# Optimization experiments

Measured on AMD Instinct MI355X. Metric: run time of the kernel, lower is better.

Reference implementation:

```python
import jax, jax.numpy as jnp
import numpy as np
from jax import lax

B, C, T, S = 32, 122, 500, 13
WID, EMB, PROJ = 80, 8, 1024
HID = 768  # (H=1)*(W=96)*(E=8) after CNN
EPS = 1e-5
DN = ('NCHW', 'OIHW', 'NCHW')


def setup_inputs() -> dict:
    key = jax.random.key(0)
    ks = jax.random.split(key, 24)
    f32 = jnp.float32
    def n(k, shape, scale):
        return (jax.random.normal(k, shape, dtype=f32) * scale).astype(f32)
    return {
        'x': jax.random.normal(ks[0], (B, C, T), dtype=f32),
        'subject_ids': jax.random.randint(ks[1], (B,), 0, S, dtype=jnp.int32),
        'W_sub': n(ks[2], (S, T, T), 0.04),      # nn.Linear(500,500) weight per subject
        'b_sub': n(ks[3], (S, T), 0.02),
        'conv1_w': n(ks[4], (WID, 1, 1, 5), 0.3),
        'conv1_b': n(ks[5], (WID,), 0.02),
        'bn1_g': 1.0 + n(ks[6], (WID,), 0.1),
        'bn1_b': n(ks[7], (WID,), 0.1),
        'bn1_m': n(ks[8], (WID,), 0.1),
        'bn1_v': 0.5 + jax.random.uniform(ks[9], (WID,), dtype=f32),
        'conv2_w': n(ks[10], (WID, WID, C, 1), 0.01),
        'conv2_b': n(ks[11], (WID,), 0.02),
        'bn2_g': 1.0 + n(ks[12], (WID,), 0.1),
        'bn2_b': n(ks[13], (WID,), 0.1),
        'bn2_m': n(ks[14], (WID,), 0.1),
        'bn2_v': 0.5 + jax.random.uniform(ks[15], (WID,), dtype=f32),
        'proj_w': n(ks[16], (EMB, WID, 1, 1), 0.1),
        'proj_b': n(ks[17], (EMB,), 0.02),
        'mlp1_w': n(ks[18], (PROJ, HID), 0.03),
        'mlp1_b': n(ks[19], (PROJ,), 0.02),
        'mlp2_w': n(ks[20], (PROJ, PROJ), 0.03),
        'mlp2_b': n(ks[21], (PROJ,), 0.02),
        'ln_g': 1.0 + n(ks[22], (PROJ,), 0.05),
        'ln_b': n(ks[23], (PROJ,), 0.05),
    }


def _bn(h, g, b, m, v):
    # eval-mode BatchNorm2d over channel axis 1
    scale = (g / jnp.sqrt(v + EPS))[None, :, None, None]
    shift = (b - m * g / jnp.sqrt(v + EPS))[None, :, None, None]
    return h * scale + shift


def _forward(x, subject_ids, W_sub, b_sub, conv1_w, conv1_b, bn1_g, bn1_b, bn1_m, bn1_v,
             conv2_w, conv2_b, bn2_g, bn2_b, bn2_m, bn2_v, proj_w, proj_b,
             mlp1_w, mlp1_b, mlp2_w, mlp2_b, ln_g, ln_b):
    # --- per-subject routing: gather each sample's Linear(500,500) and apply ---
    Wg = W_sub[subject_ids]                       # [B,T,T] (out,in)
    bg = b_sub[subject_ids]                       # [B,T]
    out = jnp.einsum('bcs,bts->bct', x, Wg) + bg[:, None, :]
    # --- spatio-temporal CNN (eval mode: dropout = identity) ---
    h = out[:, None, :, :]                        # [B,1,C,T]
    h = lax.conv_general_dilated(h, conv1_w, (1, 1), 'VALID', dimension_numbers=DN)
    h = h + conv1_b[None, :, None, None]          # [B,80,122,496]
    h = lax.reduce_window(h, 0.0, lax.add, (1, 1, 1, 17), (1, 1, 1, 5), 'VALID') / 17.0  # [B,80,122,96]
    h = jax.nn.elu(_bn(h, bn1_g, bn1_b, bn1_m, bn1_v))
    h = lax.conv_general_dilated(h, conv2_w, (1, 1), 'VALID', dimension_numbers=DN)
    h = h + conv2_b[None, :, None, None]          # [B,80,1,96]
    h = jax.nn.elu(_bn(h, bn2_g, bn2_b, bn2_m, bn2_v))
    h = lax.conv_general_dilated(h, proj_w, (1, 1), 'VALID', dimension_numbers=DN)
    h = h + proj_b[None, :, None, None]           # [B,8,1,96]
    z = jnp.transpose(h, (0, 2, 3, 1)).reshape(h.shape[0], -1)  # [B,768]
    # --- MLP projector: Linear -> Residual(GELU+Linear) -> LayerNorm ---
    z1 = z @ mlp1_w.T + mlp1_b                    # [B,1024]
    r = jax.nn.gelu(z1, approximate=False) @ mlp2_w.T + mlp2_b
    y = z1 + r
    mu = jnp.mean(y, axis=-1, keepdims=True)
    var = jnp.var(y, axis=-1, keepdims=True)
    return (y - mu) / jnp.sqrt(var + EPS) * ln_g + ln_b


def reference(x, subject_ids, W_sub, b_sub, conv1_w, conv1_b, bn1_g, bn1_b, bn1_m, bn1_v,
              conv2_w, conv2_b, bn2_g, bn2_b, bn2_m, bn2_v, proj_w, proj_b,
              mlp1_w, mlp1_b, mlp2_w, mlp2_b, ln_g, ln_b):
    return _forward(x, subject_ids, W_sub, b_sub, conv1_w, conv1_b, bn1_g, bn1_b, bn1_m, bn1_v,
                    conv2_w, conv2_b, bn2_g, bn2_b, bn2_m, bn2_v, proj_w, proj_b,
                    mlp1_w, mlp1_b, mlp2_w, mlp2_b, ln_g, ln_b)
```

## Files before the change

### kernel.cpp

```cpp
#include <hip/hip_runtime.h>
#include <math.h>

#define BB 32
#define CC 122
#define TT 500
#define SS 13
#define WID 80
#define EMB 8
#define PROJ 1024
#define HID 768
#define TP 96
#define EPSF 1e-5f
#define KP 9760
#define KSPLIT 16

typedef float f32x4 __attribute__((ext_vector_type(4)));
typedef __bf16 bf16x8 __attribute__((ext_vector_type(8)));
typedef unsigned short u16x8 __attribute__((ext_vector_type(8)));
union BF8 { u16x8 u; bf16x8 b; };

__device__ __forceinline__ unsigned short f2bf(float f) {
    union { float f; unsigned u; } v; v.f = f;
    unsigned r = v.u + 0x7FFFu + ((v.u >> 16) & 1u);
    return (unsigned short)(r >> 16);
}

__device__ __forceinline__ float eluf(float x) {
    return x > 0.f ? x : __expf(x) - 1.f;
}

#define OFF_E    ((size_t)0)
#define OFF_XB   ((size_t)1952000)
#define OFF_WB   ((size_t)3000576)
#define OFF_W2P  ((size_t)4704512)
#define OFF_PART ((size_t)20086272)
#define OFF_Z    ((size_t)24018432)
#define OFF_Z1   ((size_t)24030720)
#define OFF_G    ((size_t)24063488)
#define OFF_Y    ((size_t)24079872)
#define OFF_W1B  ((size_t)24112640)
#define OFF_W2B  ((size_t)24505856)
#define OFF_WCB  ((size_t)25030144)
#define OFF_B1F  ((size_t)25031424)
#define OFF_SC2  ((size_t)25031504)
#define OFF_SH2  ((size_t)25031584)

#define NPK_X  (2097152)
#define NPK_W  (3407872)
#define NPK_W2 (780800)
#define NPK_M1 (786432)
#define NPK_M2 (1048576)
#define NPK_TOT (NPK_X + NPK_W + NPK_W2 + NPK_M1 + NPK_M2)

__global__ __launch_bounds__(256) void k_pack(const float* __restrict__ x,
                                              const float* __restrict__ W_sub,
                                              const float* __restrict__ conv2_w,
                                              const float* __restrict__ mlp1_w,
                                              const float* __restrict__ mlp2_w,
                                              const float* __restrict__ conv1_w, const float* __restrict__ conv1_b,
                                              const float* __restrict__ g1, const float* __restrict__ b1,
                                              const float* __restrict__ m1, const float* __restrict__ v1,
                                              const float* __restrict__ conv2_b, const float* __restrict__ g2,
                                              const float* __restrict__ b2, const float* __restrict__ m2,
                                              const float* __restrict__ v2,
                                              unsigned short* __restrict__ xb,
                                              unsigned short* __restrict__ wb,
                                              unsigned short* __restrict__ w2p,
                                              unsigned short* __restrict__ w1b,
                                              unsigned short* __restrict__ w2b,
                                              unsigned short* __restrict__ wcb, float* __restrict__ bias1f,
                                              float* __restrict__ scale2, float* __restrict__ shift2f) {
    if (blockIdx.x == 0) {
        int o = threadIdx.x;
        if (o < WID) {
            float s1 = g1[o] * rsqrtf(v1[o] + EPSF);
            float sh1 = b1[o] - m1[o] * s1;
            #pragma unroll
            for (int d = 0; d < 21; d++) {
                int klo = d - 16; if (klo < 0) klo = 0;
                int khi = d;      if (khi > 4) khi = 4;
                float acc = 0.f;
                for (int k = klo; k <= khi; k++) acc += conv1_w[o*5 + k];
                wcb[o*32 + d] = f2bf(acc * s1 * (1.f/17.f));
            }
            #pragma unroll
            for (int d = 21; d < 32; d++) wcb[o*32 + d] = 0;
            bias1f[o] = conv1_b[o] * s1 + sh1;
            float s2 = g2[o] * rsqrtf(v2[o] + EPSF);
            scale2[o] = s2;
            shift2f[o] = conv2_b[o] * s2 + (b2[o] - m2[o] * s2);
        }
    }
    size_t idx = (size_t)blockIdx.x * 256 + threadIdx.x;
    if (idx >= (size_t)NPK_TOT) return;
    if (idx < NPK_X) {
        int s = idx & 511, c = (idx >> 9) & 127, b = idx >> 16;
        float v = (c < CC && s < TT) ? x[((size_t)b * CC + c) * TT + s] : 0.f;
        xb[idx] = f2bf(v);
    } else if (idx < NPK_X + NPK_W) {
        size_t j = idx - NPK_X;
        int s = j & 511, t = (j >> 9) & 511, sub = j >> 18;
        float v = (t < TT && s < TT) ? W_sub[((size_t)sub * TT + t) * TT + s] : 0.f;
        wb[j] = f2bf(v);
    } else if (idx < NPK_X + NPK_W + NPK_W2) {
        size_t j = idx - NPK_X - NPK_W;
        int o  = (int)(j / (WID * CC));
        int r  = (int)(j % (WID * CC));
        int op = r / CC, c = r % CC;
        w2p[(size_t)o * KP + (size_t)c * WID + op] = f2bf(conv2_w[j]);
    } else if (idx < NPK_X + NPK_W + NPK_W2 + NPK_M1) {
        size_t j = idx - NPK_X - NPK_W - NPK_W2;
        w1b[j] = f2bf(mlp1_w[j]);
    } else {
        size_t j = idx - NPK_X - NPK_W - NPK_W2 - NPK_M1;
        w2b[j] = f2bf(mlp2_w[j]);
    }
}

__global__ __launch_bounds__(256) void k_einsum(const unsigned short* __restrict__ xb,
                                                const unsigned short* __restrict__ wb,
                                                const int* __restrict__ sid,
                                                const float* __restrict__ b_sub,
                                                float* __restrict__ oute) {
    int t0 = blockIdx.x * 64, b = blockIdx.y;
    int s = sid[b];
    int tid = threadIdx.x, w = tid >> 6, lr = tid & 15, lg = (tid >> 4) & 3;
    const unsigned short* A0 = xb + ((size_t)(b * 128 + w * 32 + lr)) * 512 + 8 * lg;
    const unsigned short* Bb = wb + (size_t)s * 262144 + 8 * lg;
    f32x4 acc[2][4] = {};
    for (int kb = 0; kb < 512; kb += 32) {
        BF8 a0, a1;
        a0.u = *(const u16x8*)(A0 + kb);
        a1.u = *(const u16x8*)(A0 + 16 * 512 + kb);
        #pragma unroll
        for (int nt = 0; nt < 4; nt++) {
            BF8 bf; bf.u = *(const u16x8*)(Bb + (size_t)(t0 + nt * 16 + lr) * 512 + kb);
            acc[0][nt] = __builtin_amdgcn_mfma_f32_16x16x32_bf16(a0.b, bf.b, acc[0][nt], 0, 0, 0);
            acc[1][nt] = __builtin_amdgcn_mfma_f32_16x16x32_bf16(a1.b, bf.b, acc[1][nt], 0, 0, 0);
        }
    }
    const float* bg = b_sub + (size_t)s * TT;
    #pragma unroll
    for (int nt = 0; nt < 4; nt++) {
        int t = t0 + nt * 16 + lr;
        if (t < TT) {
            float bias = bg[t];
            #pragma unroll
            for (int mt = 0; mt < 2; mt++) {
                int crow = w * 32 + mt * 16 + 4 * lg;
                #pragma unroll
                for (int r = 0; r < 4; r++) {
                    int c = crow + r;
                    if (c < CC) oute[((size_t)b * CC + c) * TT + t] = acc[mt][nt][r] + bias;
                }
            }
        }
    }
}

__global__ __launch_bounds__(384) void k_fc(const float* __restrict__ oute,
                                            const unsigned short* __restrict__ wcb,
                                            const float* __restrict__ b1f,
                                            const unsigned short* __restrict__ w2p,
                                            float* __restrict__ part) {
    __shared__ float e2[2][512];
    __shared__ unsigned short pt[96][164];
    int chunk = blockIdx.x, b = blockIdx.y;
    int tid = threadIdx.x, w = tid >> 6, l = tid & 63, lr = l & 15, lg = l >> 4;
    BF8 af[5]; float4 bf4[5];
    #pragma unroll
    for (int ot = 0; ot < 5; ot++) {
        af[ot].u = *(const u16x8*)(wcb + (ot * 16 + lr) * 32 + 8 * lg);
        bf4[ot] = *(const float4*)(b1f + ot * 16 + 4 * lg);
    }
    const unsigned short* Arow = w2p + (size_t)lr * KP + 8 * lg;
    f32x4 acc2[5] = {};
    for (int ci = 0; ci < 4; ci++) {
        int cp = chunk * 4 + ci;
        bool live = cp < 61;
        if (live) {
            if (tid < 250) {
                int cc = tid / 125, i = tid % 125;
                ((float4*)e2[cc])[i] = ((const float4*)(oute + ((size_t)b * CC + cp * 2 + cc) * TT))[i];
            }
            if (tid >= 232 && tid < 256) {
                int j = tid - 232; int cc = j / 12, i = 500 + (j % 12);
                e2[cc][i] = 0.f;
            }
        }
        __syncthreads();
        if (live) {
            #pragma unroll
            for (int cc = 0; cc < 2; cc++) {
                int t = w * 16 + lr;
                const float* ew = e2[cc] + 5 * t + 8 * lg;
                BF8 bfr;
                #pragma unroll
                for (int j = 0; j < 8; j++) bfr.u[j] = f2bf(ew[j]);
                f32x4 fa[5] = {};
                #pragma unroll
                for (int ot = 0; ot < 5; ot++)
                    fa[ot] = __builtin_amdgcn_mfma_f32_16x16x32_bf16(af[ot].b, bfr.b, fa[ot], 0, 0, 0);
                #pragma unroll
                for (int ot = 0; ot < 5; ot++) {
                    union { unsigned short s[4]; uint2 v; } pk;
                    #pragma unroll
                    for (int r = 0; r < 4; r++) pk.s[r] = f2bf(eluf(fa[ot][r] + bf4[ot][r]));
                    *(uint2*)&pt[t][cc * 80 + ot * 16 + 4 * lg] = pk.v;
                }
            }
        }
        __syncthreads();
        if (live) {
            #pragma unroll
            for (int kl = 0; kl < 5; kl++) {
                BF8 bf; bf.u = *(const u16x8*)(&pt[w * 16 + lr][kl * 32 + lg * 8]);
                int ko = cp * 160 + kl * 32;
                #pragma unroll
                for (int mt = 0; mt < 5; mt++) {
                    BF8 a; a.u = *(const u16x8*)(Arow + (size_t)mt * 16 * KP + ko);
                    acc2[mt] = __builtin_amdgcn_mfma_f32_16x16x32_bf16(a.b, bf.b, acc2[mt], 0, 0, 0);
                }
            }
        }
    }
    float* pp = part + ((size_t)(chunk * BB + b) * WID) * TP;
    int t = w * 16 + lr;
    #pragma unroll
    for (int mt = 0; mt < 5; mt++) {
        int ob = mt * 16 + 4 * lg;
        #pragma unroll
        for (int r = 0; r < 4; r++)
            pp[(size_t)(ob + r) * TP + t] = acc2[mt][r];
    }
}

__global__ __launch_bounds__(256) void k_redproj(const float* __restrict__ part,
                                                 const float* __restrict__ scale2,
                                                 const float* __restrict__ shift2f,
                                                 const float* __restrict__ pw,
                                                 const float* __restrict__ pb,
                                                 unsigned short* __restrict__ zbf) {
    __shared__ float ly[WID * 24];
    __shared__ float lw[EMB * WID];
    int tq = blockIdx.x, b = blockIdx.y;
    int tid = threadIdx.x;
    int t0 = tq * 24;
    for (int i = tid; i < EMB * WID; i += 256) lw[i] = pw[i];
    for (int i = tid; i < WID * 24; i += 256) {
        int o = i / 24, tl = i % 24;
        float acc = 0.f;
        #pragma unroll
        for (int ks = 0; ks < KSPLIT; ks++)
            acc += part[(size_t)(ks * BB + b) * (WID * TP) + o * TP + t0 + tl];
        ly[o * 24 + tl] = eluf(acc * scale2[o] + shift2f[o]);
    }
    __syncthreads();
    if (tid < 24 * EMB) {
        int e = tid & 7, tl = tid >> 3;
        float acc = pb[e];
        #pragma unroll 10
        for (int o = 0; o < WID; o++) acc = fmaf(ly[o * 24 + tl], lw[e * WID + o], acc);
        zbf[(size_t)b * HID + (t0 + tl) * EMB + e] = f2bf(acc);
    }
}

__global__ __launch_bounds__(256) void k_mlp1(const unsigned short* __restrict__ zbf,
                                              const unsigned short* __restrict__ w1b,
                                              const float* __restrict__ bias,
                                              float* __restrict__ z1,
                                              unsigned short* __restrict__ gbf) {
    __shared__ float accb[2][64][4];
    int tid = threadIdx.x, w = tid >> 6, l = tid & 63, lr = l & 15, lg = l >> 4;
    int mt = w & 1, kh = w >> 1;
    int pcol = blockIdx.x * 16 + lr;
    const unsigned short* wr = w1b + (size_t)pcol * HID + kh * 384 + 8 * lg;
    const unsigned short* za = zbf + (size_t)(mt * 16 + lr) * HID + kh * 384 + 8 * lg;
    f32x4 acc = {};
    for (int kb = 0; kb < 384; kb += 32) {
        BF8 bf; bf.u = *(const u16x8*)(wr + kb);
        BF8 a;  a.u  = *(const u16x8*)(za + kb);
        acc = __builtin_amdgcn_mfma_f32_16x16x32_bf16(a.b, bf.b, acc, 0, 0, 0);
    }
    if (kh == 1) {
        #pragma unroll
        for (int r = 0; r < 4; r++) accb[mt][l][r] = acc[r];
    }
    __syncthreads();
    if (kh == 0) {
        float bs = bias[pcol];
        #pragma unroll
        for (int r = 0; r < 4; r++) {
            int row = mt * 16 + 4 * lg + r;
            float v = acc[r] + accb[mt][l][r] + bs;
            z1[(size_t)row * PROJ + pcol] = v;
            gbf[(size_t)row * PROJ + pcol] = f2bf(0.5f * v * (1.f + erff(v * 0.70710678118654752f)));
        }
    }
}

__global__ __launch_bounds__(256) void k_mlp2(const unsigned short* __restrict__ gbf,
                                              const float* __restrict__ z1,
                                              const unsigned short* __restrict__ w2b,
                                              const float* __restrict__ bias,
                                              float* __restrict__ y) {
    __shared__ float accb[2][64][4];
    int tid = threadIdx.x, w = tid >> 6, l = tid & 63, lr = l & 15, lg = l >> 4;
    int mt = w & 1, kh = w >> 1;
    int q = blockIdx.x * 16 + lr;
    const unsigned short* wr = w2b + (size_t)q * PROJ + kh * 512 + 8 * lg;
    const unsigned short* ga = gbf + (size_t)(mt * 16 + lr) * PROJ + kh * 512 + 8 * lg;
    f32x4 acc = {};
    for (int kb = 0; kb < 512; kb += 32) {
        BF8 bf; bf.u = *(const u16x8*)(wr + kb);
        BF8 a;  a.u  = *(const u16x8*)(ga + kb);
        acc = __builtin_amdgcn_mfma_f32_16x16x32_bf16(a.b, bf.b, acc, 0, 0, 0);
    }
    if (kh == 1) {
        #pragma unroll
        for (int r = 0; r < 4; r++) accb[mt][l][r] = acc[r];
    }
    __syncthreads();
    if (kh == 0) {
        float bs = bias[q];
        #pragma unroll
        for (int r = 0; r < 4; r++) {
            int row = mt * 16 + 4 * lg + r;
            y[(size_t)row * PROJ + q] = acc[r] + accb[mt][l][r] + bs + z1[(size_t)row * PROJ + q];
        }
    }
}

__global__ __launch_bounds__(256) void k_ln(const float* __restrict__ y,
                                            const float* __restrict__ lg,
                                            const float* __restrict__ lb,
                                            float* __restrict__ out) {
    int b = blockIdx.x, tid = threadIdx.x;
    const float4* yr = (const float4*)(y + (size_t)b * PROJ);
    float4 v = yr[tid];
    float s  = v.x + v.y + v.z + v.w;
    float sq = v.x*v.x + v.y*v.y + v.z*v.z + v.w*v.w;
    #pragma unroll
    for (int off = 32; off > 0; off >>= 1) {
        s  += __shfl_down(s, off);
        sq += __shfl_down(sq, off);
    }
    __shared__ float ss[4], ssq[4];
    int wv = tid >> 6, lane = tid & 63;
    if (lane == 0) { ss[wv] = s; ssq[wv] = sq; }
    __syncthreads();
    __shared__ float smu, sinv;
    if (tid == 0) {
        float Sm = ss[0] + ss[1] + ss[2] + ss[3];
        float Sq = ssq[0] + ssq[1] + ssq[2] + ssq[3];
        float mu = Sm * (1.f / PROJ);
        float var = Sq * (1.f / PROJ) - mu * mu;
        smu = mu;
        sinv = rsqrtf(var + EPSF);
    }
    __syncthreads();
    float mu = smu, inv = sinv;
    float4 g4 = ((const float4*)lg)[tid];
    float4 b4 = ((const float4*)lb)[tid];
    float4 o4;
    o4.x = (v.x - mu) * inv * g4.x + b4.x;
    o4.y = (v.y - mu) * inv * g4.y + b4.y;
    o4.z = (v.z - mu) * inv * g4.z + b4.z;
    o4.w = (v.w - mu) * inv * g4.w + b4.w;
    ((float4*)(out + (size_t)b * PROJ))[tid] = o4;
}

extern "C" void kernel_launch(void* const* d_in, const int* in_sizes, int n_in,
                              void* d_out, int out_size, void* d_ws, size_t ws_size,
                              hipStream_t stream) {
    const float* x        = (const float*)d_in[0];
    const int*   sid      = (const int*)  d_in[1];
    const float* W_sub    = (const float*)d_in[2];
    const float* b_sub    = (const float*)d_in[3];
    const float* conv1_w  = (const float*)d_in[4];
    const float* conv1_b  = (const float*)d_in[5];
    const float* bn1_g    = (const float*)d_in[6];
    const float* bn1_b    = (const float*)d_in[7];
    const float* bn1_m    = (const float*)d_in[8];
    const float* bn1_v    = (const float*)d_in[9];
    const float* conv2_w  = (const float*)d_in[10];
    const float* conv2_b  = (const float*)d_in[11];
    const float* bn2_g    = (const float*)d_in[12];
    const float* bn2_b    = (const float*)d_in[13];
    const float* bn2_m    = (const float*)d_in[14];
    const float* bn2_v    = (const float*)d_in[15];
    const float* proj_w   = (const float*)d_in[16];
    const float* proj_b   = (const float*)d_in[17];
    const float* mlp1_w   = (const float*)d_in[18];
    const float* mlp1_b   = (const float*)d_in[19];
    const float* mlp2_w   = (const float*)d_in[20];
    const float* mlp2_b   = (const float*)d_in[21];
    const float* ln_g     = (const float*)d_in[22];
    const float* ln_b     = (const float*)d_in[23];
    float* out = (float*)d_out;
    float* ws  = (float*)d_ws;

    float* ws_e    = ws + OFF_E;
    unsigned short* ws_xb  = (unsigned short*)(ws + OFF_XB);
    unsigned short* ws_wb  = (unsigned short*)(ws + OFF_WB);
    unsigned short* ws_w2p = (unsigned short*)(ws + OFF_W2P);
    float* ws_part = ws + OFF_PART;
    unsigned short* ws_zbf = (unsigned short*)(ws + OFF_Z);
    float* ws_z1   = ws + OFF_Z1;
    unsigned short* ws_gbf = (unsigned short*)(ws + OFF_G);
    float* ws_y    = ws + OFF_Y;
    unsigned short* ws_w1b = (unsigned short*)(ws + OFF_W1B);
    unsigned short* ws_w2b = (unsigned short*)(ws + OFF_W2B);
    unsigned short* ws_wcb = (unsigned short*)(ws + OFF_WCB);
    float* ws_b1f  = ws + OFF_B1F;
    float* ws_sc2  = ws + OFF_SC2;
    float* ws_sh2  = ws + OFF_SH2;

    hipLaunchKernelGGL(k_pack, dim3((NPK_TOT + 255) / 256), dim3(256), 0, stream,
                       x, W_sub, conv2_w, mlp1_w, mlp2_w,
                       conv1_w, conv1_b, bn1_g, bn1_b, bn1_m, bn1_v,
                       conv2_b, bn2_g, bn2_b, bn2_m, bn2_v,
                       ws_xb, ws_wb, ws_w2p, ws_w1b, ws_w2b,
                       ws_wcb, ws_b1f, ws_sc2, ws_sh2);

    hipLaunchKernelGGL(k_einsum, dim3(8, BB), dim3(256), 0, stream,
                       ws_xb, ws_wb, sid, b_sub, ws_e);

    hipLaunchKernelGGL(k_fc, dim3(KSPLIT, BB), dim3(384), 0, stream,
                       ws_e, ws_wcb, ws_b1f, ws_w2p, ws_part);

    hipLaunchKernelGGL(k_redproj, dim3(4, BB), dim3(256), 0, stream,
                       ws_part, ws_sc2, ws_sh2, proj_w, proj_b, ws_zbf);

    hipLaunchKernelGGL(k_mlp1, dim3(PROJ / 16), dim3(256), 0, stream,
                       ws_zbf, ws_w1b, mlp1_b, ws_z1, ws_gbf);

    hipLaunchKernelGGL(k_mlp2, dim3(PROJ / 16), dim3(256), 0, stream,
                       ws_gbf, ws_z1, ws_w2b, mlp2_b, ws_y);

    hipLaunchKernelGGL(k_ln, dim3(BB), dim3(256), 0, stream,
                       ws_y, ln_g, ln_b, out);
}
```

Before: 200.4 us.

## Fuse tail kernels into one persistent kernel with global barriers; widen einsum blocks

Replaces the four small tail launches (reduce+projection, MLP1, MLP2, LayerNorm) with a single 128-block kernel that steps through the stages, separated by atomic-counter grid barriers. The barrier counters are zeroed in the pack kernel. It also splits the MLP K dimension across four waves instead of two, and reshapes the einsum to 512 threads with one 16-row M tile per wave. The aim is to remove launch gaps between the tiny tail kernels. The cost is the spin-wait barrier, which depends on all 128 blocks being resident at once and has a timeout escape.

```diff
diff --git a/kernel.cpp b/kernel.cpp
--- a/kernel.cpp
+++ b/kernel.cpp
@@ -13,6 +13,7 @@
 #define EPSF 1e-5f
 #define KP 9760
 #define KSPLIT 16
+#define TAILBLK 128
 
 typedef float f32x4 __attribute__((ext_vector_type(4)));
 typedef __bf16 bf16x8 __attribute__((ext_vector_type(8)));
@@ -44,6 +45,7 @@
 #define OFF_B1F  ((size_t)25031424)
 #define OFF_SC2  ((size_t)25031504)
 #define OFF_SH2  ((size_t)25031584)
+#define OFF_BAR  ((size_t)25031664)
 
 #define NPK_X  (2097152)
 #define NPK_W  (3407872)
@@ -69,7 +71,8 @@
                                               unsigned short* __restrict__ w1b,
                                               unsigned short* __restrict__ w2b,
                                               unsigned short* __restrict__ wcb, float* __restrict__ bias1f,
-                                              float* __restrict__ scale2, float* __restrict__ shift2f) {
+                                              float* __restrict__ scale2, float* __restrict__ shift2f,
+                                              unsigned* __restrict__ bar) {
     if (blockIdx.x == 0) {
         int o = threadIdx.x;
         if (o < WID) {
@@ -90,6 +93,7 @@
             scale2[o] = s2;
             shift2f[o] = conv2_b[o] * s2 + (b2[o] - m2[o] * s2);
         }
+        if (o >= 96 && o < 104) bar[o - 96] = 0;
     }
     size_t idx = (size_t)blockIdx.x * 256 + threadIdx.x;
     if (idx >= (size_t)NPK_TOT) return;
@@ -117,7 +121,7 @@
     }
 }
 
-__global__ __launch_bounds__(256) void k_einsum(const unsigned short* __restrict__ xb,
+__global__ __launch_bounds__(512) void k_einsum(const unsigned short* __restrict__ xb,
                                                 const unsigned short* __restrict__ wb,
                                                 const int* __restrict__ sid,
                                                 const float* __restrict__ b_sub,
@@ -125,18 +129,16 @@
     int t0 = blockIdx.x * 64, b = blockIdx.y;
     int s = sid[b];
     int tid = threadIdx.x, w = tid >> 6, lr = tid & 15, lg = (tid >> 4) & 3;
-    const unsigned short* A0 = xb + ((size_t)(b * 128 + w * 32 + lr)) * 512 + 8 * lg;
+    const unsigned short* A0 = xb + ((size_t)(b * 128 + w * 16 + lr)) * 512 + 8 * lg;
     const unsigned short* Bb = wb + (size_t)s * 262144 + 8 * lg;
-    f32x4 acc[2][4] = {};
+    f32x4 acc[4] = {};
     for (int kb = 0; kb < 512; kb += 32) {
-        BF8 a0, a1;
+        BF8 a0;
         a0.u = *(const u16x8*)(A0 + kb);
-        a1.u = *(const u16x8*)(A0 + 16 * 512 + kb);
         #pragma unroll
         for (int nt = 0; nt < 4; nt++) {
             BF8 bf; bf.u = *(const u16x8*)(Bb + (size_t)(t0 + nt * 16 + lr) * 512 + kb);
-            acc[0][nt] = __builtin_amdgcn_mfma_f32_16x16x32_bf16(a0.b, bf.b, acc[0][nt], 0, 0, 0);
-            acc[1][nt] = __builtin_amdgcn_mfma_f32_16x16x32_bf16(a1.b, bf.b, acc[1][nt], 0, 0, 0);
+            acc[nt] = __builtin_amdgcn_mfma_f32_16x16x32_bf16(a0.b, bf.b, acc[nt], 0, 0, 0);
         }
     }
     const float* bg = b_sub + (size_t)s * TT;
@@ -145,14 +147,11 @@
         int t = t0 + nt * 16 + lr;
         if (t < TT) {
             float bias = bg[t];
-            #pragma unroll
-            for (int mt = 0; mt < 2; mt++) {
-                int crow = w * 32 + mt * 16 + 4 * lg;
-                #pragma unroll
-                for (int r = 0; r < 4; r++) {
-                    int c = crow + r;
-                    if (c < CC) oute[((size_t)b * CC + c) * TT + t] = acc[mt][nt][r] + bias;
-                }
+            int crow = w * 16 + 4 * lg;
+            #pragma unroll
+            for (int r = 0; r < 4; r++) {
+                int c = crow + r;
+                if (c < CC) oute[((size_t)b * CC + c) * TT + t] = acc[nt][r] + bias;
             }
         }
     }
@@ -235,139 +234,162 @@
     }
 }
 
-__global__ __launch_bounds__(256) void k_redproj(const float* __restrict__ part,
-                                                 const float* __restrict__ scale2,
-                                                 const float* __restrict__ shift2f,
-                                                 const float* __restrict__ pw,
-                                                 const float* __restrict__ pb,
-                                                 unsigned short* __restrict__ zbf) {
-    __shared__ float ly[WID * 24];
-    __shared__ float lw[EMB * WID];
-    int tq = blockIdx.x, b = blockIdx.y;
-    int tid = threadIdx.x;
-    int t0 = tq * 24;
-    for (int i = tid; i < EMB * WID; i += 256) lw[i] = pw[i];
-    for (int i = tid; i < WID * 24; i += 256) {
-        int o = i / 24, tl = i % 24;
-        float acc = 0.f;
-        #pragma unroll
-        for (int ks = 0; ks < KSPLIT; ks++)
-            acc += part[(size_t)(ks * BB + b) * (WID * TP) + o * TP + t0 + tl];
-        ly[o * 24 + tl] = eluf(acc * scale2[o] + shift2f[o]);
-    }
+__device__ __forceinline__ void gbar(unsigned* c, unsigned target) {
     __syncthreads();
-    if (tid < 24 * EMB) {
-        int e = tid & 7, tl = tid >> 3;
-        float acc = pb[e];
-        #pragma unroll 10
-        for (int o = 0; o < WID; o++) acc = fmaf(ly[o * 24 + tl], lw[e * WID + o], acc);
-        zbf[(size_t)b * HID + (t0 + tl) * EMB + e] = f2bf(acc);
-    }
-}
-
-__global__ __launch_bounds__(256) void k_mlp1(const unsigned short* __restrict__ zbf,
+    if (threadIdx.x == 0) {
+        __threadfence();
+        atomicAdd(c, 1u);
+        long long t0 = clock64();
+        while (__hip_atomic_load(c, __ATOMIC_ACQUIRE, __HIP_MEMORY_SCOPE_AGENT) < target) {
+            if (clock64() - t0 > 300000000LL) break;
+        }
+        __threadfence();
+    }
+    __syncthreads();
+}
+
+__global__ __launch_bounds__(256) void k_tail(const float* __restrict__ part,
+                                              const float* __restrict__ sc2,
+                                              const float* __restrict__ sh2,
+                                              const float* __restrict__ pw,
+                                              const float* __restrict__ pb,
                                               const unsigned short* __restrict__ w1b,
-                                              const float* __restrict__ bias,
+                                              const float* __restrict__ m1bias,
+                                              const unsigned short* __restrict__ w2b,
+                                              const float* __restrict__ m2bias,
+                                              const float* __restrict__ lngw,
+                                              const float* __restrict__ lnbw,
+                                              unsigned short* __restrict__ zbf,
                                               float* __restrict__ z1,
-                                              unsigned short* __restrict__ gbf) {
-    __shared__ float accb[2][64][4];
-    int tid = threadIdx.x, w = tid >> 6, l = tid & 63, lr = l & 15, lg = l >> 4;
-    int mt = w & 1, kh = w >> 1;
-    int pcol = blockIdx.x * 16 + lr;
-    const unsigned short* wr = w1b + (size_t)pcol * HID + kh * 384 + 8 * lg;
-    const unsigned short* za = zbf + (size_t)(mt * 16 + lr) * HID + kh * 384 + 8 * lg;
-    f32x4 acc = {};
-    for (int kb = 0; kb < 384; kb += 32) {
-        BF8 bf; bf.u = *(const u16x8*)(wr + kb);
-        BF8 a;  a.u  = *(const u16x8*)(za + kb);
-        acc = __builtin_amdgcn_mfma_f32_16x16x32_bf16(a.b, bf.b, acc, 0, 0, 0);
-    }
-    if (kh == 1) {
-        #pragma unroll
-        for (int r = 0; r < 4; r++) accb[mt][l][r] = acc[r];
-    }
-    __syncthreads();
-    if (kh == 0) {
-        float bs = bias[pcol];
-        #pragma unroll
-        for (int r = 0; r < 4; r++) {
-            int row = mt * 16 + 4 * lg + r;
-            float v = acc[r] + accb[mt][l][r] + bs;
-            z1[(size_t)row * PROJ + pcol] = v;
-            gbf[(size_t)row * PROJ + pcol] = f2bf(0.5f * v * (1.f + erff(v * 0.70710678118654752f)));
-        }
-    }
-}
-
-__global__ __launch_bounds__(256) void k_mlp2(const unsigned short* __restrict__ gbf,
-                                              const float* __restrict__ z1,
-                                              const unsigned short* __restrict__ w2b,
-                                              const float* __restrict__ bias,
-                                              float* __restrict__ y) {
-    __shared__ float accb[2][64][4];
-    int tid = threadIdx.x, w = tid >> 6, l = tid & 63, lr = l & 15, lg = l >> 4;
-    int mt = w & 1, kh = w >> 1;
-    int q = blockIdx.x * 16 + lr;
-    const unsigned short* wr = w2b + (size_t)q * PROJ + kh * 512 + 8 * lg;
-    const unsigned short* ga = gbf + (size_t)(mt * 16 + lr) * PROJ + kh * 512 + 8 * lg;
-    f32x4 acc = {};
-    for (int kb = 0; kb < 512; kb += 32) {
-        BF8 bf; bf.u = *(const u16x8*)(wr + kb);
-        BF8 a;  a.u  = *(const u16x8*)(ga + kb);
-        acc = __builtin_amdgcn_mfma_f32_16x16x32_bf16(a.b, bf.b, acc, 0, 0, 0);
-    }
-    if (kh == 1) {
-        #pragma unroll
-        for (int r = 0; r < 4; r++) accb[mt][l][r] = acc[r];
-    }
-    __syncthreads();
-    if (kh == 0) {
-        float bs = bias[q];
-        #pragma unroll
-        for (int r = 0; r < 4; r++) {
-            int row = mt * 16 + 4 * lg + r;
-            y[(size_t)row * PROJ + q] = acc[r] + accb[mt][l][r] + bs + z1[(size_t)row * PROJ + q];
-        }
-    }
-}
-
-__global__ __launch_bounds__(256) void k_ln(const float* __restrict__ y,
-                                            const float* __restrict__ lg,
-                                            const float* __restrict__ lb,
-                                            float* __restrict__ out) {
-    int b = blockIdx.x, tid = threadIdx.x;
-    const float4* yr = (const float4*)(y + (size_t)b * PROJ);
-    float4 v = yr[tid];
-    float s  = v.x + v.y + v.z + v.w;
-    float sq = v.x*v.x + v.y*v.y + v.z*v.z + v.w*v.w;
-    #pragma unroll
-    for (int off = 32; off > 0; off >>= 1) {
-        s  += __shfl_down(s, off);
-        sq += __shfl_down(sq, off);
-    }
-    __shared__ float ss[4], ssq[4];
-    int wv = tid >> 6, lane = tid & 63;
-    if (lane == 0) { ss[wv] = s; ssq[wv] = sq; }
-    __syncthreads();
-    __shared__ float smu, sinv;
-    if (tid == 0) {
-        float Sm = ss[0] + ss[1] + ss[2] + ss[3];
-        float Sq = ssq[0] + ssq[1] + ssq[2] + ssq[3];
-        float mu = Sm * (1.f / PROJ);
-        float var = Sq * (1.f / PROJ) - mu * mu;
-        smu = mu;
-        sinv = rsqrtf(var + EPSF);
-    }
-    __syncthreads();
-    float mu = smu, inv = sinv;
-    float4 g4 = ((const float4*)lg)[tid];
-    float4 b4 = ((const float4*)lb)[tid];
-    float4 o4;
-    o4.x = (v.x - mu) * inv * g4.x + b4.x;
-    o4.y = (v.y - mu) * inv * g4.y + b4.y;
-    o4.z = (v.z - mu) * inv * g4.z + b4.z;
-    o4.w = (v.w - mu) * inv * g4.w + b4.w;
-    ((float4*)(out + (size_t)b * PROJ))[tid] = o4;
+                                              unsigned short* __restrict__ gbf,
+                                              float* __restrict__ y,
+                                              unsigned* __restrict__ bar,
+                                              float* __restrict__ out) {
+    __shared__ union {
+        struct { float ly[WID * 24]; float lw[EMB * WID]; } rp;
+        float accb[4][64][4];
+        struct { float ss[4]; float ssq[4]; float smu; float sinv; } ln;
+    } sm;
+    const int bid = blockIdx.x;
+    const int tid = threadIdx.x;
+
+    {
+        int tq = bid >> 5, b = bid & 31;
+        int t0 = tq * 24;
+        for (int i = tid; i < EMB * WID; i += 256) sm.rp.lw[i] = pw[i];
+        for (int i = tid; i < WID * 24; i += 256) {
+            int o = i / 24, tl = i - o * 24;
+            float acc = 0.f;
+            #pragma unroll
+            for (int ks = 0; ks < KSPLIT; ks++)
+                acc += part[(size_t)(ks * BB + b) * (WID * TP) + o * TP + t0 + tl];
+            sm.rp.ly[o * 24 + tl] = eluf(acc * sc2[o] + sh2[o]);
+        }
+        __syncthreads();
+        if (tid < 24 * EMB) {
+            int e = tid & 7, tl = tid >> 3;
+            float acc = pb[e];
+            #pragma unroll 10
+            for (int o = 0; o < WID; o++) acc = fmaf(sm.rp.ly[o * 24 + tl], sm.rp.lw[e * WID + o], acc);
+            zbf[(size_t)b * HID + (t0 + tl) * EMB + e] = f2bf(acc);
+        }
+    }
+    gbar(bar + 0, TAILBLK);
+
+    {
+        int cu = bid >> 1, rh = bid & 1;
+        int w = tid >> 6, l = tid & 63, lr = l & 15, lg = l >> 4;
+        int pcol = cu * 16 + lr;
+        const unsigned short* wr = w1b + (size_t)pcol * HID + w * 192 + 8 * lg;
+        const unsigned short* za = zbf + (size_t)(rh * 16 + lr) * HID + w * 192 + 8 * lg;
+        f32x4 acc = {};
+        #pragma unroll
+        for (int kb = 0; kb < 192; kb += 32) {
+            BF8 bf; bf.u = *(const u16x8*)(wr + kb);
+            BF8 a;  a.u  = *(const u16x8*)(za + kb);
+            acc = __builtin_amdgcn_mfma_f32_16x16x32_bf16(a.b, bf.b, acc, 0, 0, 0);
+        }
+        #pragma unroll
+        for (int r = 0; r < 4; r++) sm.accb[w][l][r] = acc[r];
+        __syncthreads();
+        if (w == 0) {
+            float bs = m1bias[pcol];
+            #pragma unroll
+            for (int r = 0; r < 4; r++) {
+                int row = rh * 16 + 4 * lg + r;
+                float v = bs;
+                #pragma unroll
+                for (int q = 0; q < 4; q++) v += sm.accb[q][l][r];
+                z1[(size_t)row * PROJ + pcol] = v;
+                gbf[(size_t)row * PROJ + pcol] = f2bf(0.5f * v * (1.f + erff(v * 0.70710678118654752f)));
+            }
+        }
+    }
+    gbar(bar + 1, TAILBLK);
+
+    {
+        int cu = bid >> 1, rh = bid & 1;
+        int w = tid >> 6, l = tid & 63, lr = l & 15, lg = l >> 4;
+        int pc = cu * 16 + lr;
+        const unsigned short* wr = w2b + (size_t)pc * PROJ + w * 256 + 8 * lg;
+        const unsigned short* ga = gbf + (size_t)(rh * 16 + lr) * PROJ + w * 256 + 8 * lg;
+        f32x4 acc = {};
+        #pragma unroll
+        for (int kb = 0; kb < 256; kb += 32) {
+            BF8 bf; bf.u = *(const u16x8*)(wr + kb);
+            BF8 a;  a.u  = *(const u16x8*)(ga + kb);
+            acc = __builtin_amdgcn_mfma_f32_16x16x32_bf16(a.b, bf.b, acc, 0, 0, 0);
+        }
+        #pragma unroll
+        for (int r = 0; r < 4; r++) sm.accb[w][l][r] = acc[r];
+        __syncthreads();
+        if (w == 0) {
+            float bs = m2bias[pc];
+            #pragma unroll
+            for (int r = 0; r < 4; r++) {
+                int row = rh * 16 + 4 * lg + r;
+                float v = bs + z1[(size_t)row * PROJ + pc];
+                #pragma unroll
+                for (int q = 0; q < 4; q++) v += sm.accb[q][l][r];
+                y[(size_t)row * PROJ + pc] = v;
+            }
+        }
+    }
+    gbar(bar + 2, TAILBLK);
+
+    if (bid < BB) {
+        int b = bid;
+        const float4* yr = (const float4*)(y + (size_t)b * PROJ);
+        float4 v = yr[tid];
+        float s  = v.x + v.y + v.z + v.w;
+        float sq = v.x*v.x + v.y*v.y + v.z*v.z + v.w*v.w;
+        #pragma unroll
+        for (int off = 32; off > 0; off >>= 1) {
+            s  += __shfl_down(s, off);
+            sq += __shfl_down(sq, off);
+        }
+        int wv = tid >> 6, lane = tid & 63;
+        if (lane == 0) { sm.ln.ss[wv] = s; sm.ln.ssq[wv] = sq; }
+        __syncthreads();
+        if (tid == 0) {
+            float Sm = sm.ln.ss[0] + sm.ln.ss[1] + sm.ln.ss[2] + sm.ln.ss[3];
+            float Sq = sm.ln.ssq[0] + sm.ln.ssq[1] + sm.ln.ssq[2] + sm.ln.ssq[3];
+            float mu = Sm * (1.f / PROJ);
+            float var = Sq * (1.f / PROJ) - mu * mu;
+            sm.ln.smu = mu;
+            sm.ln.sinv = rsqrtf(var + EPSF);
+        }
+        __syncthreads();
+        float mu = sm.ln.smu, inv = sm.ln.sinv;
+        float4 g4 = ((const float4*)lngw)[tid];
+        float4 b4 = ((const float4*)lnbw)[tid];
+        float4 o4;
+        o4.x = (v.x - mu) * inv * g4.x + b4.x;
+        o4.y = (v.y - mu) * inv * g4.y + b4.y;
+        o4.z = (v.z - mu) * inv * g4.z + b4.z;
+        o4.w = (v.w - mu) * inv * g4.w + b4.w;
+        ((float4*)(out + (size_t)b * PROJ))[tid] = o4;
+    }
 }
 
 extern "C" void kernel_launch(void* const* d_in, const int* in_sizes, int n_in,
@@ -415,29 +437,23 @@
     float* ws_b1f  = ws + OFF_B1F;
     float* ws_sc2  = ws + OFF_SC2;
     float* ws_sh2  = ws + OFF_SH2;
+    unsigned* ws_bar = (unsigned*)(ws + OFF_BAR);
 
     hipLaunchKernelGGL(k_pack, dim3((NPK_TOT + 255) / 256), dim3(256), 0, stream,
                        x, W_sub, conv2_w, mlp1_w, mlp2_w,
                        conv1_w, conv1_b, bn1_g, bn1_b, bn1_m, bn1_v,
                        conv2_b, bn2_g, bn2_b, bn2_m, bn2_v,
                        ws_xb, ws_wb, ws_w2p, ws_w1b, ws_w2b,
-                       ws_wcb, ws_b1f, ws_sc2, ws_sh2);
-
-    hipLaunchKernelGGL(k_einsum, dim3(8, BB), dim3(256), 0, stream,
+                       ws_wcb, ws_b1f, ws_sc2, ws_sh2, ws_bar);
+
+    hipLaunchKernelGGL(k_einsum, dim3(8, BB), dim3(512), 0, stream,
                        ws_xb, ws_wb, sid, b_sub, ws_e);
 
     hipLaunchKernelGGL(k_fc, dim3(KSPLIT, BB), dim3(384), 0, stream,
                        ws_e, ws_wcb, ws_b1f, ws_w2p, ws_part);
 
-    hipLaunchKernelGGL(k_redproj, dim3(4, BB), dim3(256), 0, stream,
-                       ws_part, ws_sc2, ws_sh2, proj_w, proj_b, ws_zbf);
-
-    hipLaunchKernelGGL(k_mlp1, dim3(PROJ / 16), dim3(256), 0, stream,
-                       ws_zbf, ws_w1b, mlp1_b, ws_z1, ws_gbf);
-
-    hipLaunchKernelGGL(k_mlp2, dim3(PROJ / 16), dim3(256), 0, stream,
-                       ws_gbf, ws_z1, ws_w2b, mlp2_b, ws_y);
-
-    hipLaunchKernelGGL(k_ln, dim3(BB), dim3(256), 0, stream,
-                       ws_y, ln_g, ln_b, out);
-}
+    hipLaunchKernelGGL(k_tail, dim3(TAILBLK), dim3(256), 0, stream,
+                       ws_part, ws_sc2, ws_sh2, proj_w, proj_b,
+                       ws_w1b, mlp1_b, ws_w2b, mlp2_b, ln_g, ln_b,
+                       ws_zbf, ws_z1, ws_gbf, ws_y, ws_bar, out);
+}
```

Result: slower. 223.4 us (+11.5%).

## Split einsum, reduce/project and MLP kernels into more blocks for parallelism

Applied to the files above, without the earlier changes.

Halves the time tile of the subject einsum (twice as many blocks), halves the time slice per k_redproj block and vectorizes its split-K reduction with float4 loads, and reorganizes both MLP GEMMs so each block handles one 16-row half with a 4-way K split across waves reduced via shared memory. The aim is to fill more compute units on a small batch problem where grids were tiny (64 blocks for the MLPs). In exchange, B-operand reuse per block drops in the einsum and MLP weights are read by two blocks each.

```diff
diff --git a/kernel.cpp b/kernel.cpp
--- a/kernel.cpp
+++ b/kernel.cpp
@@ -122,18 +122,18 @@
                                                 const int* __restrict__ sid,
                                                 const float* __restrict__ b_sub,
                                                 float* __restrict__ oute) {
-    int t0 = blockIdx.x * 64, b = blockIdx.y;
+    int t0 = blockIdx.x * 32, b = blockIdx.y;
     int s = sid[b];
     int tid = threadIdx.x, w = tid >> 6, lr = tid & 15, lg = (tid >> 4) & 3;
     const unsigned short* A0 = xb + ((size_t)(b * 128 + w * 32 + lr)) * 512 + 8 * lg;
     const unsigned short* Bb = wb + (size_t)s * 262144 + 8 * lg;
-    f32x4 acc[2][4] = {};
+    f32x4 acc[2][2] = {};
     for (int kb = 0; kb < 512; kb += 32) {
         BF8 a0, a1;
         a0.u = *(const u16x8*)(A0 + kb);
         a1.u = *(const u16x8*)(A0 + 16 * 512 + kb);
         #pragma unroll
-        for (int nt = 0; nt < 4; nt++) {
+        for (int nt = 0; nt < 2; nt++) {
             BF8 bf; bf.u = *(const u16x8*)(Bb + (size_t)(t0 + nt * 16 + lr) * 512 + kb);
             acc[0][nt] = __builtin_amdgcn_mfma_f32_16x16x32_bf16(a0.b, bf.b, acc[0][nt], 0, 0, 0);
             acc[1][nt] = __builtin_amdgcn_mfma_f32_16x16x32_bf16(a1.b, bf.b, acc[1][nt], 0, 0, 0);
@@ -141,7 +141,7 @@
     }
     const float* bg = b_sub + (size_t)s * TT;
     #pragma unroll
-    for (int nt = 0; nt < 4; nt++) {
+    for (int nt = 0; nt < 2; nt++) {
         int t = t0 + nt * 16 + lr;
         if (t < TT) {
             float bias = bg[t];
@@ -241,26 +241,33 @@
                                                  const float* __restrict__ pw,
                                                  const float* __restrict__ pb,
                                                  unsigned short* __restrict__ zbf) {
-    __shared__ float ly[WID * 24];
+    __shared__ float ly[WID * 12];
     __shared__ float lw[EMB * WID];
     int tq = blockIdx.x, b = blockIdx.y;
     int tid = threadIdx.x;
-    int t0 = tq * 24;
+    int t0 = tq * 12;
     for (int i = tid; i < EMB * WID; i += 256) lw[i] = pw[i];
-    for (int i = tid; i < WID * 24; i += 256) {
-        int o = i / 24, tl = i % 24;
-        float acc = 0.f;
+    if (tid < 240) {
+        int o = tid / 3, q = tid % 3;
+        const float* pbase = part + (size_t)b * (WID * TP) + o * TP + t0 + 4 * q;
+        float4 a = {0.f, 0.f, 0.f, 0.f};
         #pragma unroll
-        for (int ks = 0; ks < KSPLIT; ks++)
-            acc += part[(size_t)(ks * BB + b) * (WID * TP) + o * TP + t0 + tl];
-        ly[o * 24 + tl] = eluf(acc * scale2[o] + shift2f[o]);
+        for (int ks = 0; ks < KSPLIT; ks++) {
+            float4 v = *(const float4*)(pbase + (size_t)ks * (BB * WID * TP));
+            a.x += v.x; a.y += v.y; a.z += v.z; a.w += v.w;
+        }
+        float sc = scale2[o], sh = shift2f[o];
+        ly[o * 12 + 4 * q + 0] = eluf(a.x * sc + sh);
+        ly[o * 12 + 4 * q + 1] = eluf(a.y * sc + sh);
+        ly[o * 12 + 4 * q + 2] = eluf(a.z * sc + sh);
+        ly[o * 12 + 4 * q + 3] = eluf(a.w * sc + sh);
     }
     __syncthreads();
-    if (tid < 24 * EMB) {
+    if (tid < 12 * EMB) {
         int e = tid & 7, tl = tid >> 3;
         float acc = pb[e];
         #pragma unroll 10
-        for (int o = 0; o < WID; o++) acc = fmaf(ly[o * 24 + tl], lw[e * WID + o], acc);
+        for (int o = 0; o < WID; o++) acc = fmaf(ly[o * 12 + tl], lw[e * WID + o], acc);
         zbf[(size_t)b * HID + (t0 + tl) * EMB + e] = f2bf(acc);
     }
 }
@@ -270,29 +277,30 @@
                                               const float* __restrict__ bias,
                                               float* __restrict__ z1,
                                               unsigned short* __restrict__ gbf) {
-    __shared__ float accb[2][64][4];
+    __shared__ float accb[4][64][4];
+    int cu = blockIdx.x >> 1, rh = blockIdx.x & 1;
     int tid = threadIdx.x, w = tid >> 6, l = tid & 63, lr = l & 15, lg = l >> 4;
-    int mt = w & 1, kh = w >> 1;
-    int pcol = blockIdx.x * 16 + lr;
-    const unsigned short* wr = w1b + (size_t)pcol * HID + kh * 384 + 8 * lg;
-    const unsigned short* za = zbf + (size_t)(mt * 16 + lr) * HID + kh * 384 + 8 * lg;
+    int pcol = cu * 16 + lr;
+    const unsigned short* wr = w1b + (size_t)pcol * HID + w * 192 + 8 * lg;
+    const unsigned short* za = zbf + (size_t)(rh * 16 + lr) * HID + w * 192 + 8 * lg;
     f32x4 acc = {};
-    for (int kb = 0; kb < 384; kb += 32) {
+    #pragma unroll
+    for (int kb = 0; kb < 192; kb += 32) {
         BF8 bf; bf.u = *(const u16x8*)(wr + kb);
         BF8 a;  a.u  = *(const u16x8*)(za + kb);
         acc = __builtin_amdgcn_mfma_f32_16x16x32_bf16(a.b, bf.b, acc, 0, 0, 0);
     }
-    if (kh == 1) {
-        #pragma unroll
-        for (int r = 0; r < 4; r++) accb[mt][l][r] = acc[r];
-    }
+    #pragma unroll
+    for (int r = 0; r < 4; r++) accb[w][l][r] = acc[r];
     __syncthreads();
-    if (kh == 0) {
+    if (w == 0) {
         float bs = bias[pcol];
         #pragma unroll
         for (int r = 0; r < 4; r++) {
-            int row = mt * 16 + 4 * lg + r;
-            float v = acc[r] + accb[mt][l][r] + bs;
+            int row = rh * 16 + 4 * lg + r;
+            float v = bs;
+            #pragma unroll
+            for (int q = 0; q < 4; q++) v += accb[q][l][r];
             z1[(size_t)row * PROJ + pcol] = v;
             gbf[(size_t)row * PROJ + pcol] = f2bf(0.5f * v * (1.f + erff(v * 0.70710678118654752f)));
         }
@@ -304,29 +312,31 @@
                                               const unsigned short* __restrict__ w2b,
                                               const float* __restrict__ bias,
                                               float* __restrict__ y) {
-    __shared__ float accb[2][64][4];
+    __shared__ float accb[4][64][4];
+    int cu = blockIdx.x >> 1, rh = blockIdx.x & 1;
     int tid = threadIdx.x, w = tid >> 6, l = tid & 63, lr = l & 15, lg = l >> 4;
-    int mt = w & 1, kh = w >> 1;
-    int q = blockIdx.x * 16 + lr;
-    const unsigned short* wr = w2b + (size_t)q * PROJ + kh * 512 + 8 * lg;
-    const unsigned short* ga = gbf + (size_t)(mt * 16 + lr) * PROJ + kh * 512 + 8 * lg;
+    int pc = cu * 16 + lr;
+    const unsigned short* wr = w2b + (size_t)pc * PROJ + w * 256 + 8 * lg;
+    const unsigned short* ga = gbf + (size_t)(rh * 16 + lr) * PROJ + w * 256 + 8 * lg;
     f32x4 acc = {};
-    for (int kb = 0; kb < 512; kb += 32) {
+    #pragma unroll
+    for (int kb = 0; kb < 256; kb += 32) {
         BF8 bf; bf.u = *(const u16x8*)(wr + kb);
         BF8 a;  a.u  = *(const u16x8*)(ga + kb);
         acc = __builtin_amdgcn_mfma_f32_16x16x32_bf16(a.b, bf.b, acc, 0, 0, 0);
     }
-    if (kh == 1) {
-        #pragma unroll
-        for (int r = 0; r < 4; r++) accb[mt][l][r] = acc[r];
-    }
+    #pragma unroll
+    for (int r = 0; r < 4; r++) accb[w][l][r] = acc[r];
     __syncthreads();
-    if (kh == 0) {
-        float bs = bias[q];
+    if (w == 0) {
+        float bs = bias[pc];
         #pragma unroll
         for (int r = 0; r < 4; r++) {
-            int row = mt * 16 + 4 * lg + r;
-            y[(size_t)row * PROJ + q] = acc[r] + accb[mt][l][r] + bs + z1[(size_t)row * PROJ + q];
+            int row = rh * 16 + 4 * lg + r;
+            float v = bs + z1[(size_t)row * PROJ + pc];
+            #pragma unroll
+            for (int q = 0; q < 4; q++) v += accb[q][l][r];
+            y[(size_t)row * PROJ + pc] = v;
         }
     }
 }
@@ -423,19 +433,19 @@
                        ws_xb, ws_wb, ws_w2p, ws_w1b, ws_w2b,
                        ws_wcb, ws_b1f, ws_sc2, ws_sh2);
 
-    hipLaunchKernelGGL(k_einsum, dim3(8, BB), dim3(256), 0, stream,
+    hipLaunchKernelGGL(k_einsum, dim3(16, BB), dim3(256), 0, stream,
                        ws_xb, ws_wb, sid, b_sub, ws_e);
 
     hipLaunchKernelGGL(k_fc, dim3(KSPLIT, BB), dim3(384), 0, stream,
                        ws_e, ws_wcb, ws_b1f, ws_w2p, ws_part);
 
-    hipLaunchKernelGGL(k_redproj, dim3(4, BB), dim3(256), 0, stream,
+    hipLaunchKernelGGL(k_redproj, dim3(8, BB), dim3(256), 0, stream,
                        ws_part, ws_sc2, ws_sh2, proj_w, proj_b, ws_zbf);
 
-    hipLaunchKernelGGL(k_mlp1, dim3(PROJ / 16), dim3(256), 0, stream,
+    hipLaunchKernelGGL(k_mlp1, dim3(128), dim3(256), 0, stream,
                        ws_zbf, ws_w1b, mlp1_b, ws_z1, ws_gbf);
 
-    hipLaunchKernelGGL(k_mlp2, dim3(PROJ / 16), dim3(256), 0, stream,
+    hipLaunchKernelGGL(k_mlp2, dim3(128), dim3(256), 0, stream,
                        ws_gbf, ws_z1, ws_w2b, mlp2_b, ws_y);
 
     hipLaunchKernelGGL(k_ln, dim3(BB), dim3(256), 0, stream,
```

Measured after the change: 200.7 us. About the same (+0.2%).
